# Performance work log

Measured on AMD Instinct MI355X. Metric: run time of the kernel, lower is better.

## Reference

```python
import jax, jax.numpy as jnp
import numpy as np

N, E, G, H, L, GD = 100000, 1600000, 64, 128, 3, 32
NEG_SLOPE = 0.2
EPS = 1e-5


def setup_inputs() -> dict:
    key = jax.random.key(0)
    ks = jax.random.split(key, 10)
    s = 1.0 / np.sqrt(H)
    return {
        "x": jax.random.normal(ks[0], (N, H), jnp.float32),
        "global_feat": jax.random.normal(ks[1], (G, GD), jnp.float32),
        "W_src": jax.random.normal(ks[2], (L, H, H), jnp.float32) * s,
        "W_dst": jax.random.normal(ks[3], (L, H, H), jnp.float32) * s,
        "att": jax.random.normal(ks[4], (L, H), jnp.float32) * s,
        "b_conv": jnp.zeros((L, H), jnp.float32),
        "gn_w": jnp.ones((L, H), jnp.float32),
        "gn_b": jnp.zeros((L, H), jnp.float32),
        "gn_ms": jnp.ones((L, H), jnp.float32),
        "W1": jax.random.normal(ks[5], (H * L + GD, H), jnp.float32) * (1.0 / np.sqrt(H * L + GD)),
        "b1": jnp.zeros((H,), jnp.float32),
        "W2": jax.random.normal(ks[6], (H, 1), jnp.float32) * s,
        "b2": jnp.zeros((1,), jnp.float32),
        "edge_index": jax.random.randint(ks[7], (2, E), 0, N, jnp.int64),
        "batch": jnp.sort(jax.random.randint(ks[8], (N,), 0, G, jnp.int64)),
    }


def reference(x, global_feat, W_src, W_dst, att, b_conv, gn_w, gn_b, gn_ms,
              W1, b1, W2, b2, edge_index, batch):
    n = x.shape[0]
    g = global_feat.shape[0]
    layers = W_src.shape[0]
    loops = jnp.arange(n, dtype=edge_index.dtype)
    src = jnp.concatenate([edge_index[0], loops])  # add_self_loops=True
    dst = jnp.concatenate([edge_index[1], loops])
    counts = jnp.maximum(
        jax.ops.segment_sum(jnp.ones((n,), x.dtype), batch, num_segments=g), 1.0)

    outs = []
    for l in range(layers):
        # --- GATv2Conv (heads=1) ---
        xl = x @ W_src[l]          # source transform [N,H]
        xr = x @ W_dst[l]          # target transform [N,H]
        e = jax.nn.leaky_relu(xl[src] + xr[dst], NEG_SLOPE) @ att[l]  # [Etot]
        emax = jax.ops.segment_max(e, dst, num_segments=n)
        ex = jnp.exp(e - emax[dst])
        denom = jax.ops.segment_sum(ex, dst, num_segments=n)
        alpha = ex / denom[dst]
        h = jax.ops.segment_sum(alpha[:, None] * xl[src], dst, num_segments=n) + b_conv[l]
        # --- GraphNorm ---
        mean = jax.ops.segment_sum(h, batch, num_segments=g) / counts[:, None]
        sub = h - gn_ms[l] * mean[batch]
        var = jax.ops.segment_sum(sub * sub, batch, num_segments=g) / counts[:, None]
        h = gn_w[l] * sub * jax.lax.rsqrt(var[batch] + EPS) + gn_b[l]
        x = jax.nn.relu(h)
        # --- global_mean_pool ---
        outs.append(jax.ops.segment_sum(x, batch, num_segments=g) / counts[:, None])

    hcat = jnp.concatenate(outs + [global_feat], axis=1)  # JK cat + global feats
    z = jax.nn.relu(hcat @ W1 + b1)  # dropout = identity (eval)
    return z @ W2 + b2
```

## Files before the change

### kernel.cpp

```cpp
#include <hip/hip_runtime.h>
#include <hip/hip_bf16.h>
#include <math.h>

#define N_    100000
#define E_    1600000
#define ETOT_ 1700000
#define G_    64
#define H_    128
#define GH_   8192
#define L_    3
#define GD_   32
#define NEG_  0.2f
#define EPS_  1e-5f

#define NBUK_ 391
#define CH_   2048
#define MCH_  782

typedef unsigned short ushort_t;
typedef unsigned int uint_t;
typedef __attribute__((ext_vector_type(4))) float f32x4;
typedef __attribute__((ext_vector_type(8))) short bf16x8;
typedef __attribute__((ext_vector_type(8))) unsigned short ushort8;

__device__ __forceinline__ ushort_t bfb(float f) {
    __hip_bfloat16 h = __float2bfloat16(f);
    return *reinterpret_cast<ushort_t*>(&h);
}
__device__ __forceinline__ uint_t pack_bf2(float a, float b) {
    return (uint_t)bfb(a) | ((uint_t)bfb(b) << 16);
}
__device__ __forceinline__ float uf(ushort_t u) {
    return __uint_as_float(((uint_t)u) << 16);
}


__global__ void k_init(float* pooled, float* gsum, float* gsq, int* gstart,
                       const int* __restrict__ batch,
                       const float* __restrict__ Ws, const float* __restrict__ Wd,
                       ushort_t* __restrict__ Wt) {
    int i = blockIdx.x * 256 + threadIdx.x;
    if (i < L_ * GH_) { pooled[i] = 0.f; gsum[i] = 0.f; gsq[i] = 0.f; }
    if (i <= G_) {
        int lo = 0, hi = N_;
        while (lo < hi) { int mid = (lo + hi) >> 1; if (batch[mid] < i) lo = mid + 1; else hi = mid; }
        gstart[i] = lo;
    }
    if (i < L_ * 256 * H_) {
        int l = i >> 15;
        int r = i & 32767;
        int c = r >> 7, k = r & 127;
        float v = (c < H_) ? Ws[(size_t)l * H_ * H_ + k * H_ + c]
                           : Wd[(size_t)l * H_ * H_ + k * H_ + (c - H_)];
        Wt[i] = bfb(v);
    }
}


__global__ __launch_bounds__(256) void k_bcount(const int* __restrict__ edst, int* __restrict__ C) {
    __shared__ int hist[NBUK_];
    int t = threadIdx.x, m = blockIdx.x;
    for (int i = t; i < NBUK_; i += 256) hist[i] = 0;
    __syncthreads();
    int base = m * CH_;
#pragma unroll
    for (int j = 0; j < CH_ / 256; j++) {
        int e = base + j * 256 + t;
        if (e < E_) atomicAdd(&hist[edst[e] >> 8], 1);
    }
    __syncthreads();
    for (int i = t; i < NBUK_; i += 256) C[i * MCH_ + m] = hist[i];
}

__global__ __launch_bounds__(1024) void k_bscan(int* __restrict__ C, int* __restrict__ bucketEdges) {
    __shared__ int arr[1024];
    int b = blockIdx.x, t = threadIdx.x;
    int v = (t < MCH_) ? C[b * MCH_ + t] : 0;
    arr[t] = v;
    __syncthreads();
    for (int off = 1; off < 1024; off <<= 1) {
        int x = (t >= off) ? arr[t - off] : 0;
        __syncthreads();
        arr[t] += x;
        __syncthreads();
    }
    if (t < MCH_) C[b * MCH_ + t] = arr[t] - v;
    if (t == 1023) bucketEdges[b] = arr[1023];
}

__global__ __launch_bounds__(512) void k_bscan2(const int* __restrict__ bucketEdges,
                                                int* __restrict__ bstartE, int* __restrict__ bstartT,
                                                int* __restrict__ rowptr) {
    __shared__ int aE[512], aT[512];
    int t = threadIdx.x;
    int e = 0, tot = 0;
    if (t < NBUK_) {
        e = bucketEdges[t];
        int nib = N_ - t * 256; if (nib > 256) nib = 256;
        tot = e + nib;
    }
    aE[t] = e; aT[t] = tot;
    __syncthreads();
    for (int off = 1; off < 512; off <<= 1) {
        int xe = (t >= off) ? aE[t - off] : 0;
        int xt = (t >= off) ? aT[t - off] : 0;
        __syncthreads();
        aE[t] += xe; aT[t] += xt;
        __syncthreads();
    }
    if (t < NBUK_) { bstartE[t] = aE[t] - e; bstartT[t] = aT[t] - tot; }
    if (t == 0) rowptr[N_] = ETOT_;
}

__global__ __launch_bounds__(256) void k_bscatter(const int* __restrict__ esrc, const int* __restrict__ edst,
                                                  const int* __restrict__ C, const int* __restrict__ bstartE,
                                                  uint_t* __restrict__ stag) {
    __shared__ int cur[NBUK_];
    int t = threadIdx.x, m = blockIdx.x;
    for (int i = t; i < NBUK_; i += 256) cur[i] = C[i * MCH_ + m] + bstartE[i];
    __syncthreads();
    int base = m * CH_;
#pragma unroll
    for (int j = 0; j < CH_ / 256; j++) {
        int e = base + j * 256 + t;
        if (e < E_) {
            int s = esrc[e], d = edst[e];
            int pos = atomicAdd(&cur[d >> 8], 1);
            stag[pos] = ((uint_t)s << 8) | (uint_t)(d & 255);
        }
    }
}

__global__ __launch_bounds__(256) void k_bfinal(const uint_t* __restrict__ stag,
                                                const int* __restrict__ bucketEdges,
                                                const int* __restrict__ bstartE, const int* __restrict__ bstartT,
                                                int* __restrict__ rowptr, int* __restrict__ colarr) {
    __shared__ int deg[256];
    __shared__ int cursor[256];
    int b = blockIdx.x, t = threadIdx.x;
    int nb0 = b * 256;
    int nib = N_ - nb0; if (nib > 256) nib = 256;
    int ebeg = bstartE[b], ecnt = bucketEdges[b];
    deg[t] = (t < nib) ? 1 : 0;
    __syncthreads();
    for (int i = t; i < ecnt; i += 256) {
        uint_t p = stag[ebeg + i];
        atomicAdd(&deg[p & 255u], 1);
    }
    __syncthreads();
    int v = deg[t];
    cursor[t] = v;
    __syncthreads();
    for (int off = 1; off < 256; off <<= 1) {
        int x = (t >= off) ? cursor[t - off] : 0;
        __syncthreads();
        cursor[t] += x;
        __syncthreads();
    }
    int excl = cursor[t] - v;
    int rowbase = bstartT[b];
    if (t < nib) {
        rowptr[nb0 + t] = rowbase + excl;
        colarr[rowbase + excl] = nb0 + t;
    }
    __syncthreads();
    cursor[t] = excl + 1;
    __syncthreads();
    for (int i = t; i < ecnt; i += 256) {
        uint_t p = stag[ebeg + i];
        int pos = atomicAdd(&cursor[p & 255u], 1);
        colarr[rowbase + pos] = (int)(p >> 8);
    }
}


template<int FIRST>
__global__ __launch_bounds__(256) void k_mfma_t(const float* __restrict__ x0,
                                                const ushort_t* __restrict__ hin,
                                                const int* __restrict__ batch,
                                                const float* __restrict__ mv,
                                                const float* __restrict__ iv,
                                                const float* __restrict__ bb,
                                                const ushort_t* __restrict__ Wt,
                                                ushort_t* __restrict__ xlb,
                                                ushort_t* __restrict__ xrb) {
    int wv = threadIdx.x >> 6, lane = threadIdx.x & 63;
    int row0 = (blockIdx.x * 4 + wv) * 16;
    if (row0 >= N_) return;
    int sl = lane & 15, q = lane >> 4;
    int row = row0 + sl;

    bf16x8 bx[4];
    if (FIRST) {
        const float* ap = x0 + (size_t)row * H_ + q * 8;
#pragma unroll
        for (int kk = 0; kk < 4; kk++) {
            float4 v0 = *(const float4*)(ap + kk * 32);
            float4 v1 = *(const float4*)(ap + kk * 32 + 4);
            bf16x8 t;
            t[0] = (short)bfb(v0.x); t[1] = (short)bfb(v0.y);
            t[2] = (short)bfb(v0.z); t[3] = (short)bfb(v0.w);
            t[4] = (short)bfb(v1.x); t[5] = (short)bfb(v1.y);
            t[6] = (short)bfb(v1.z); t[7] = (short)bfb(v1.w);
            bx[kk] = t;
        }
    } else {
        int g = batch[row];
        const ushort_t* hp = hin + (size_t)row * H_ + q * 8;
        const float* mvp = mv + g * H_ + q * 8;
        const float* ivp = iv + g * H_ + q * 8;
        const float* bbp = bb + q * 8;
#pragma unroll
        for (int kk = 0; kk < 4; kk++) {
            ushort8 u = *(const ushort8*)(hp + kk * 32);
            float4 m0 = *(const float4*)(mvp + kk * 32);
            float4 m1 = *(const float4*)(mvp + kk * 32 + 4);
            float4 i0 = *(const float4*)(ivp + kk * 32);
            float4 i1 = *(const float4*)(ivp + kk * 32 + 4);
            float4 c0 = *(const float4*)(bbp + kk * 32);
            float4 c1 = *(const float4*)(bbp + kk * 32 + 4);
            bf16x8 t;
            t[0] = (short)bfb(fmaxf((uf(u[0]) - m0.x) * i0.x + c0.x, 0.f));
            t[1] = (short)bfb(fmaxf((uf(u[1]) - m0.y) * i0.y + c0.y, 0.f));
            t[2] = (short)bfb(fmaxf((uf(u[2]) - m0.z) * i0.z + c0.z, 0.f));
            t[3] = (short)bfb(fmaxf((uf(u[3]) - m0.w) * i0.w + c0.w, 0.f));
            t[4] = (short)bfb(fmaxf((uf(u[4]) - m1.x) * i1.x + c1.x, 0.f));
            t[5] = (short)bfb(fmaxf((uf(u[5]) - m1.y) * i1.y + c1.y, 0.f));
            t[6] = (short)bfb(fmaxf((uf(u[6]) - m1.z) * i1.z + c1.z, 0.f));
            t[7] = (short)bfb(fmaxf((uf(u[7]) - m1.w) * i1.w + c1.w, 0.f));
            bx[kk] = t;
        }
    }

    f32x4 acc[16];
#pragma unroll
    for (int c = 0; c < 16; c++) acc[c] = (f32x4){0.f, 0.f, 0.f, 0.f};

#pragma unroll
    for (int c = 0; c < 16; c++) {
        const ushort_t* wp = Wt + (size_t)(c * 16 + sl) * H_ + q * 8;
#pragma unroll
        for (int kk = 0; kk < 4; kk++) {
            bf16x8 aw = *(const bf16x8*)(wp + kk * 32);
            acc[c] = __builtin_amdgcn_mfma_f32_16x16x32_bf16(aw, bx[kk], acc[c], 0, 0, 0);
        }
    }

    ushort_t* xlp = xlb + (size_t)row * H_ + q * 4;
    ushort_t* xrp = xrb + (size_t)row * H_ + q * 4;
#pragma unroll
    for (int c = 0; c < 8; c++) {
        uint2 o;
        o.x = pack_bf2(acc[c][0], acc[c][1]);
        o.y = pack_bf2(acc[c][2], acc[c][3]);
        *(uint2*)(xlp + c * 16) = o;
    }
#pragma unroll
    for (int c = 8; c < 16; c++) {
        uint2 o;
        o.x = pack_bf2(acc[c][0], acc[c][1]);
        o.y = pack_bf2(acc[c][2], acc[c][3]);
        *(uint2*)(xrp + (c - 8) * 16) = o;
    }
}


__global__ __launch_bounds__(256) void k_conv(const ushort_t* __restrict__ xlb,
                                              const ushort_t* __restrict__ xrb,
                                              const int* __restrict__ rowptr,
                                              const int* __restrict__ colarr,
                                              const float* __restrict__ attl, const float* __restrict__ bcl,
                                              ushort_t* __restrict__ h) {
    int tid = threadIdx.x;
    int lane = tid & 63, wv = tid >> 6;
    int sl = lane & 15, q = lane >> 4;
    int row = blockIdx.x * 16 + wv * 4 + q;
    int d0 = sl * 8;

    float xrv[8], av[8], av5[8];
    {
        ushort8 ux = *(const ushort8*)(xrb + (size_t)row * H_ + d0);
        float4 a0 = *(const float4*)(attl + d0);
        float4 a1 = *(const float4*)(attl + d0 + 4);
        av[0] = a0.x; av[1] = a0.y; av[2] = a0.z; av[3] = a0.w;
        av[4] = a1.x; av[5] = a1.y; av[6] = a1.z; av[7] = a1.w;
#pragma unroll
        for (int e = 0; e < 8; e++) { xrv[e] = uf(ux[e]); av5[e] = NEG_ * av[e]; }
    }

    int jb = rowptr[row];
    int n = rowptr[row + 1] - jb;

    float ssum0 = 0.f, ssum1 = 0.f;
    float ac0[8] = {0.f, 0.f, 0.f, 0.f, 0.f, 0.f, 0.f, 0.f};
    float ac1[8] = {0.f, 0.f, 0.f, 0.f, 0.f, 0.f, 0.f, 0.f};

    auto PROC = [&](const ushort8& u, float& ss, float* acm) {
        float v[8];
        float p = 0.f;
#pragma unroll
        for (int e = 0; e < 8; e++) {
            v[e] = uf(u[e]);
            float t = v[e] + xrv[e];
            p = fmaf(t, (t > 0.f ? av[e] : av5[e]), p);
        }
        p += __shfl_xor(p, 8);
        p += __shfl_xor(p, 4);
        p += __shfl_xor(p, 2);
        p += __shfl_xor(p, 1);
        float wgt = __expf(p);
        ss += wgt;
#pragma unroll
        for (int e = 0; e < 8; e++) acm[e] = fmaf(wgt, v[e], acm[e]);
    };

    int cA = colarr[jb];
    ushort8 uA = *(const ushort8*)(xlb + (size_t)cA * H_ + d0);
    int cB = colarr[jb + (n > 1 ? 1 : 0)];
    ushort8 uB = *(const ushort8*)(xlb + (size_t)cB * H_ + d0);

    int i = 0;
    for (; i + 2 < n; i += 2) {
        int cC = colarr[jb + i + 2];
        int cD = colarr[jb + (i + 3 < n ? i + 3 : i + 2)];
        PROC(uA, ssum0, ac0);
        uA = *(const ushort8*)(xlb + (size_t)cC * H_ + d0);
        PROC(uB, ssum1, ac1);
        uB = *(const ushort8*)(xlb + (size_t)cD * H_ + d0);
    }
    PROC(uA, ssum0, ac0);
    if (i + 1 < n) PROC(uB, ssum1, ac1);

    float inv = 1.f / (ssum0 + ssum1);
    float4 b0 = *(const float4*)(bcl + d0);
    float4 b1 = *(const float4*)(bcl + d0 + 4);
    ushort8 ho;
    ho[0] = bfb((ac0[0] + ac1[0]) * inv + b0.x); ho[1] = bfb((ac0[1] + ac1[1]) * inv + b0.y);
    ho[2] = bfb((ac0[2] + ac1[2]) * inv + b0.z); ho[3] = bfb((ac0[3] + ac1[3]) * inv + b0.w);
    ho[4] = bfb((ac0[4] + ac1[4]) * inv + b1.x); ho[5] = bfb((ac0[5] + ac1[5]) * inv + b1.y);
    ho[6] = bfb((ac0[6] + ac1[6]) * inv + b1.z); ho[7] = bfb((ac0[7] + ac1[7]) * inv + b1.w);
    *(ushort8*)(h + (size_t)row * H_ + d0) = ho;
}


__global__ void k_gn_stat(const ushort_t* __restrict__ h, const int* __restrict__ batch,
                          float* gsum, float* gsq) {
    int tid = threadIdx.x;
    int nb = blockIdx.x * 64;
    int d2 = (tid & 63) * 2, hh = tid >> 6;
    int nend = nb + 64; if (nend > N_) nend = N_;
    float s10 = 0.f, s11 = 0.f, s20 = 0.f, s21 = 0.f; int curg = -1;
    for (int n = nb + hh; n < nend; n += 4) {
        int g = batch[n];
        if (g != curg) {
            if (curg >= 0) {
                atomicAdd(&gsum[curg * H_ + d2], s10);
                atomicAdd(&gsum[curg * H_ + d2 + 1], s11);
                atomicAdd(&gsq[curg * H_ + d2], s20);
                atomicAdd(&gsq[curg * H_ + d2 + 1], s21);
            }
            s10 = s11 = s20 = s21 = 0.f; curg = g;
        }
        uint_t u = *(const uint_t*)(h + (size_t)n * H_ + d2);
        float v0 = __uint_as_float(u << 16);
        float v1 = __uint_as_float(u & 0xffff0000u);
        s10 += v0; s11 += v1; s20 += v0 * v0; s21 += v1 * v1;
    }
    if (curg >= 0) {
        atomicAdd(&gsum[curg * H_ + d2], s10);
        atomicAdd(&gsum[curg * H_ + d2 + 1], s11);
        atomicAdd(&gsq[curg * H_ + d2], s20);
        atomicAdd(&gsq[curg * H_ + d2 + 1], s21);
    }
}


__global__ void k_gn_fin(float* gsum, float* gsq, const int* __restrict__ gstart,
                         const float* __restrict__ gnwl, const float* __restrict__ gnmsl) {
    int i = blockIdx.x * 256 + threadIdx.x;
    if (i < GH_) {
        int g = i >> 7, d = i & 127;
        int c = gstart[g + 1] - gstart[g]; if (c < 1) c = 1;
        float ic = 1.f / (float)c;
        float mean = gsum[i] * ic;
        float e2   = gsq[i] * ic;
        float ms = gnmsl[d];
        float var = e2 - ms * (2.f - ms) * mean * mean;
        gsum[i] = ms * mean;
        gsq[i]  = gnwl[d] * rsqrtf(var + EPS_);
    }
}


__global__ void k_pool(const ushort_t* __restrict__ h, const int* __restrict__ batch,
                       const float* __restrict__ mv, const float* __restrict__ iv,
                       const float* __restrict__ bb, float* __restrict__ pooled_l) {
    int tid = threadIdx.x;
    int nb = blockIdx.x * 64;
    int d2 = (tid & 63) * 2, hh = tid >> 6;
    int nend = nb + 64; if (nend > N_) nend = N_;
    float b0 = bb[d2], b1 = bb[d2 + 1];
    float p0 = 0.f, p1 = 0.f; int curg = -1;
    float m0 = 0.f, m1 = 0.f, i0 = 0.f, i1 = 0.f;
    for (int n = nb + hh; n < nend; n += 4) {
        int g = batch[n];
        if (g != curg) {
            if (curg >= 0) {
                atomicAdd(&pooled_l[curg * H_ + d2], p0);
                atomicAdd(&pooled_l[curg * H_ + d2 + 1], p1);
            }
            p0 = 0.f; p1 = 0.f; curg = g;
            m0 = mv[g * H_ + d2]; m1 = mv[g * H_ + d2 + 1];
            i0 = iv[g * H_ + d2]; i1 = iv[g * H_ + d2 + 1];
        }
        uint_t u = *(const uint_t*)(h + (size_t)n * H_ + d2);
        float v0 = __uint_as_float(u << 16);
        float v1 = __uint_as_float(u & 0xffff0000u);
        v0 = fmaxf((v0 - m0) * i0 + b0, 0.f);
        v1 = fmaxf((v1 - m1) * i1 + b1, 0.f);
        p0 += v0; p1 += v1;
    }
    if (curg >= 0) {
        atomicAdd(&pooled_l[curg * H_ + d2], p0);
        atomicAdd(&pooled_l[curg * H_ + d2 + 1], p1);
    }
}


__global__ __launch_bounds__(128) void k_mlp(const float* __restrict__ pooled, const float* __restrict__ gfeat,
                                             const int* __restrict__ gstart,
                                             const float* __restrict__ W1, const float* __restrict__ b1,
                                             const float* __restrict__ W2, const float* __restrict__ b2,
                                             float* __restrict__ out) {
    int g = blockIdx.x;
    int c = threadIdx.x;
    __shared__ float hc[H_ * L_ + GD_];
    __shared__ float zz[H_];
    int cn = gstart[g + 1] - gstart[g]; if (cn < 1) cn = 1;
    float ic = 1.f / (float)cn;
    for (int k = c; k < H_ * L_; k += 128)
        hc[k] = pooled[(k >> 7) * GH_ + g * H_ + (k & 127)] * ic;
    if (c < GD_) hc[H_ * L_ + c] = gfeat[g * GD_ + c];
    __syncthreads();
    float z = b1[c];
#pragma unroll 4
    for (int k = 0; k < H_ * L_ + GD_; k++)
        z += hc[k] * W1[k * H_ + c];
    z = fmaxf(z, 0.f);
    zz[c] = z * W2[c];
    __syncthreads();
    for (int off = 64; off > 0; off >>= 1) {
        if (c < off) zz[c] += zz[c + off];
        __syncthreads();
    }
    if (c == 0) out[g] = zz[0] + b2[0];
}


extern "C" void kernel_launch(void* const* d_in, const int* in_sizes, int n_in,
                              void* d_out, int out_size, void* d_ws, size_t ws_size,
                              hipStream_t stream) {
    const float* x0    = (const float*)d_in[0];
    const float* gfeat = (const float*)d_in[1];
    const float* Wsrc  = (const float*)d_in[2];
    const float* Wdst  = (const float*)d_in[3];
    const float* att   = (const float*)d_in[4];
    const float* bconv = (const float*)d_in[5];
    const float* gnw   = (const float*)d_in[6];
    const float* gnb   = (const float*)d_in[7];
    const float* gnms  = (const float*)d_in[8];
    const float* W1    = (const float*)d_in[9];
    const float* b1    = (const float*)d_in[10];
    const float* W2    = (const float*)d_in[11];
    const float* b2    = (const float*)d_in[12];
    const int*   eidx  = (const int*)d_in[13];
    const int*   batch = (const int*)d_in[14];
    const int* esrc = eidx;
    const int* edst = eidx + E_;
    float* out = (float*)d_out;

    char* w = (char*)d_ws;
    size_t off = 0;
    auto alloc = [&](size_t bytes) { char* p = w + off; off += (bytes + 255) & ~(size_t)255; return p; };
    ushort_t* xlb  = (ushort_t*)alloc((size_t)N_ * H_ * 2);
    ushort_t* xrb  = (ushort_t*)alloc((size_t)N_ * H_ * 2);
    ushort_t* h    = (ushort_t*)alloc((size_t)N_ * H_ * 2);
    ushort_t* Wt   = (ushort_t*)alloc((size_t)L_ * 256 * H_ * 2);
    int*   rowptr  = (int*)alloc((size_t)(N_ + 1) * 4);
    int*   colarr  = (int*)alloc((size_t)ETOT_ * 4);
    int*   bktE    = (int*)alloc(NBUK_ * 4);
    int*   bstartE = (int*)alloc(NBUK_ * 4);
    int*   bstartT = (int*)alloc(NBUK_ * 4);
    int*   gstart  = (int*)alloc((G_ + 1) * 4);
    float* gsum    = (float*)alloc((size_t)L_ * GH_ * 4);
    float* gsq     = (float*)alloc((size_t)L_ * GH_ * 4);
    float* pooled  = (float*)alloc((size_t)L_ * GH_ * 4);
    uint_t* stag = (uint_t*)xlb;
    int*    C    = (int*)xrb;
    (void)ws_size; (void)in_sizes; (void)n_in; (void)out_size;

    k_init<<<(N_ + 255) / 256, 256, 0, stream>>>(pooled, gsum, gsq, gstart, batch,
                                                 Wsrc, Wdst, Wt);
    k_bcount<<<MCH_, 256, 0, stream>>>(edst, C);
    k_bscan<<<NBUK_, 1024, 0, stream>>>(C, bktE);
    k_bscan2<<<1, 512, 0, stream>>>(bktE, bstartE, bstartT, rowptr);
    k_bscatter<<<MCH_, 256, 0, stream>>>(esrc, edst, C, bstartE, stag);
    k_bfinal<<<NBUK_, 256, 0, stream>>>(stag, bktE, bstartE, bstartT, rowptr, colarr);

    int mfma_grid = (N_ / 16 + 3) / 4;
    for (int l = 0; l < L_; l++) {
        if (l == 0)
            k_mfma_t<1><<<mfma_grid, 256, 0, stream>>>(x0, h, batch, gsum, gsq, gnb,
                                                       Wt, xlb, xrb);
        else
            k_mfma_t<0><<<mfma_grid, 256, 0, stream>>>(x0, h, batch,
                                                       gsum + (size_t)(l - 1) * GH_,
                                                       gsq + (size_t)(l - 1) * GH_,
                                                       gnb + (size_t)(l - 1) * H_,
                                                       Wt + (size_t)l * 256 * H_, xlb, xrb);
        k_conv<<<N_ / 16, 256, 0, stream>>>(xlb, xrb, rowptr, colarr,
                                            att + (size_t)l * H_, bconv + (size_t)l * H_, h);
        k_gn_stat<<<(N_ + 63) / 64, 256, 0, stream>>>(h, batch,
                                                      gsum + (size_t)l * GH_, gsq + (size_t)l * GH_);
        k_gn_fin<<<GH_ / 256, 256, 0, stream>>>(gsum + (size_t)l * GH_, gsq + (size_t)l * GH_,
                                                gstart, gnw + (size_t)l * H_, gnms + (size_t)l * H_);
        k_pool<<<(N_ + 63) / 64, 256, 0, stream>>>(h, batch,
                                                   gsum + (size_t)l * GH_, gsq + (size_t)l * GH_,
                                                   gnb + (size_t)l * H_, pooled + (size_t)l * GH_);
    }

    k_mlp<<<G_, 128, 0, stream>>>(pooled, gfeat, gstart, W1, b1, W2, b2, out);
}
```

Measured before the change: 684.2 us.

## Switch intermediates to fp16 and use packed half math in the edge conv

Stores the projected features, the weights and the conv output in fp16 instead of bf16, and uses f16 MFMA for the projection. The edge-attention kernel now does leaky-relu, attention dot product and weighted accumulation with packed fp16 vector arithmetic instead of per-element fp32. Its two-accumulator unrolled gather is replaced by a single-accumulator loop with a three-deep software prefetch. This cuts ALU work per edge, but accumulating in fp16 risks precision loss and overflow, and the single accumulator lengthens the dependency chain.

```diff
diff --git a/kernel.cpp b/kernel.cpp
--- a/kernel.cpp
+++ b/kernel.cpp
@@ -1,5 +1,4 @@
 #include <hip/hip_runtime.h>
-#include <hip/hip_bf16.h>
 #include <math.h>
 
 #define N_    100000
@@ -19,19 +18,19 @@
 
 typedef unsigned short ushort_t;
 typedef unsigned int uint_t;
+typedef _Float16 half_t;
 typedef __attribute__((ext_vector_type(4))) float f32x4;
-typedef __attribute__((ext_vector_type(8))) short bf16x8;
-typedef __attribute__((ext_vector_type(8))) unsigned short ushort8;
-
-__device__ __forceinline__ ushort_t bfb(float f) {
-    __hip_bfloat16 h = __float2bfloat16(f);
+typedef __attribute__((ext_vector_type(2))) _Float16 h2;
+typedef __attribute__((ext_vector_type(8))) _Float16 f16x8;
+
+__device__ __forceinline__ ushort_t hbits(float f) {
+    half_t h = (half_t)f;
     return *reinterpret_cast<ushort_t*>(&h);
 }
-__device__ __forceinline__ uint_t pack_bf2(float a, float b) {
-    return (uint_t)bfb(a) | ((uint_t)bfb(b) << 16);
-}
-__device__ __forceinline__ float uf(ushort_t u) {
-    return __uint_as_float(((uint_t)u) << 16);
+__device__ __forceinline__ uint_t pack_h2(float a, float b) {
+    half_t ha = (half_t)a, hb = (half_t)b;
+    return (uint_t)*reinterpret_cast<ushort_t*>(&ha) |
+           ((uint_t)*reinterpret_cast<ushort_t*>(&hb) << 16);
 }
 
 
@@ -52,7 +51,7 @@
         int c = r >> 7, k = r & 127;
         float v = (c < H_) ? Ws[(size_t)l * H_ * H_ + k * H_ + c]
                            : Wd[(size_t)l * H_ * H_ + k * H_ + (c - H_)];
-        Wt[i] = bfb(v);
+        Wt[i] = hbits(v);
     }
 }
 
@@ -190,18 +189,18 @@
     int sl = lane & 15, q = lane >> 4;
     int row = row0 + sl;
 
-    bf16x8 bx[4];
+    f16x8 bx[4];
     if (FIRST) {
         const float* ap = x0 + (size_t)row * H_ + q * 8;
 #pragma unroll
         for (int kk = 0; kk < 4; kk++) {
             float4 v0 = *(const float4*)(ap + kk * 32);
             float4 v1 = *(const float4*)(ap + kk * 32 + 4);
-            bf16x8 t;
-            t[0] = (short)bfb(v0.x); t[1] = (short)bfb(v0.y);
-            t[2] = (short)bfb(v0.z); t[3] = (short)bfb(v0.w);
-            t[4] = (short)bfb(v1.x); t[5] = (short)bfb(v1.y);
-            t[6] = (short)bfb(v1.z); t[7] = (short)bfb(v1.w);
+            f16x8 t;
+            t[0] = (half_t)v0.x; t[1] = (half_t)v0.y;
+            t[2] = (half_t)v0.z; t[3] = (half_t)v0.w;
+            t[4] = (half_t)v1.x; t[5] = (half_t)v1.y;
+            t[6] = (half_t)v1.z; t[7] = (half_t)v1.w;
             bx[kk] = t;
         }
     } else {
@@ -212,22 +211,22 @@
         const float* bbp = bb + q * 8;
 #pragma unroll
         for (int kk = 0; kk < 4; kk++) {
-            ushort8 u = *(const ushort8*)(hp + kk * 32);
+            f16x8 u = *(const f16x8*)(hp + kk * 32);
             float4 m0 = *(const float4*)(mvp + kk * 32);
             float4 m1 = *(const float4*)(mvp + kk * 32 + 4);
             float4 i0 = *(const float4*)(ivp + kk * 32);
             float4 i1 = *(const float4*)(ivp + kk * 32 + 4);
             float4 c0 = *(const float4*)(bbp + kk * 32);
             float4 c1 = *(const float4*)(bbp + kk * 32 + 4);
-            bf16x8 t;
-            t[0] = (short)bfb(fmaxf((uf(u[0]) - m0.x) * i0.x + c0.x, 0.f));
-            t[1] = (short)bfb(fmaxf((uf(u[1]) - m0.y) * i0.y + c0.y, 0.f));
-            t[2] = (short)bfb(fmaxf((uf(u[2]) - m0.z) * i0.z + c0.z, 0.f));
-            t[3] = (short)bfb(fmaxf((uf(u[3]) - m0.w) * i0.w + c0.w, 0.f));
-            t[4] = (short)bfb(fmaxf((uf(u[4]) - m1.x) * i1.x + c1.x, 0.f));
-            t[5] = (short)bfb(fmaxf((uf(u[5]) - m1.y) * i1.y + c1.y, 0.f));
-            t[6] = (short)bfb(fmaxf((uf(u[6]) - m1.z) * i1.z + c1.z, 0.f));
-            t[7] = (short)bfb(fmaxf((uf(u[7]) - m1.w) * i1.w + c1.w, 0.f));
+            f16x8 t;
+            t[0] = (half_t)fmaxf(((float)u[0] - m0.x) * i0.x + c0.x, 0.f);
+            t[1] = (half_t)fmaxf(((float)u[1] - m0.y) * i0.y + c0.y, 0.f);
+            t[2] = (half_t)fmaxf(((float)u[2] - m0.z) * i0.z + c0.z, 0.f);
+            t[3] = (half_t)fmaxf(((float)u[3] - m0.w) * i0.w + c0.w, 0.f);
+            t[4] = (half_t)fmaxf(((float)u[4] - m1.x) * i1.x + c1.x, 0.f);
+            t[5] = (half_t)fmaxf(((float)u[5] - m1.y) * i1.y + c1.y, 0.f);
+            t[6] = (half_t)fmaxf(((float)u[6] - m1.z) * i1.z + c1.z, 0.f);
+            t[7] = (half_t)fmaxf(((float)u[7] - m1.w) * i1.w + c1.w, 0.f);
             bx[kk] = t;
         }
     }
@@ -241,8 +240,8 @@
         const ushort_t* wp = Wt + (size_t)(c * 16 + sl) * H_ + q * 8;
 #pragma unroll
         for (int kk = 0; kk < 4; kk++) {
-            bf16x8 aw = *(const bf16x8*)(wp + kk * 32);
-            acc[c] = __builtin_amdgcn_mfma_f32_16x16x32_bf16(aw, bx[kk], acc[c], 0, 0, 0);
+            f16x8 aw = *(const f16x8*)(wp + kk * 32);
+            acc[c] = __builtin_amdgcn_mfma_f32_16x16x32_f16(aw, bx[kk], acc[c], 0, 0, 0);
         }
     }
 
@@ -251,15 +250,15 @@
 #pragma unroll
     for (int c = 0; c < 8; c++) {
         uint2 o;
-        o.x = pack_bf2(acc[c][0], acc[c][1]);
-        o.y = pack_bf2(acc[c][2], acc[c][3]);
+        o.x = pack_h2(acc[c][0], acc[c][1]);
+        o.y = pack_h2(acc[c][2], acc[c][3]);
         *(uint2*)(xlp + c * 16) = o;
     }
 #pragma unroll
     for (int c = 8; c < 16; c++) {
         uint2 o;
-        o.x = pack_bf2(acc[c][0], acc[c][1]);
-        o.y = pack_bf2(acc[c][2], acc[c][3]);
+        o.x = pack_h2(acc[c][0], acc[c][1]);
+        o.y = pack_h2(acc[c][2], acc[c][3]);
         *(uint2*)(xrp + (c - 8) * 16) = o;
     }
 }
@@ -277,69 +276,64 @@
     int row = blockIdx.x * 16 + wv * 4 + q;
     int d0 = sl * 8;
 
-    float xrv[8], av[8], av5[8];
+    const half_t neg = (half_t)NEG_;
+    f16x8 xr8 = *(const f16x8*)(xrb + (size_t)row * H_ + d0);
+    f16x8 at8;
     {
-        ushort8 ux = *(const ushort8*)(xrb + (size_t)row * H_ + d0);
         float4 a0 = *(const float4*)(attl + d0);
         float4 a1 = *(const float4*)(attl + d0 + 4);
-        av[0] = a0.x; av[1] = a0.y; av[2] = a0.z; av[3] = a0.w;
-        av[4] = a1.x; av[5] = a1.y; av[6] = a1.z; av[7] = a1.w;
-#pragma unroll
-        for (int e = 0; e < 8; e++) { xrv[e] = uf(ux[e]); av5[e] = NEG_ * av[e]; }
+        at8[0] = (half_t)a0.x; at8[1] = (half_t)a0.y;
+        at8[2] = (half_t)a0.z; at8[3] = (half_t)a0.w;
+        at8[4] = (half_t)a1.x; at8[5] = (half_t)a1.y;
+        at8[6] = (half_t)a1.z; at8[7] = (half_t)a1.w;
     }
 
     int jb = rowptr[row];
     int n = rowptr[row + 1] - jb;
-
-    float ssum0 = 0.f, ssum1 = 0.f;
-    float ac0[8] = {0.f, 0.f, 0.f, 0.f, 0.f, 0.f, 0.f, 0.f};
-    float ac1[8] = {0.f, 0.f, 0.f, 0.f, 0.f, 0.f, 0.f, 0.f};
-
-    auto PROC = [&](const ushort8& u, float& ss, float* acm) {
-        float v[8];
-        float p = 0.f;
-#pragma unroll
-        for (int e = 0; e < 8; e++) {
-            v[e] = uf(u[e]);
-            float t = v[e] + xrv[e];
-            p = fmaf(t, (t > 0.f ? av[e] : av5[e]), p);
-        }
+    int last = n - 1;
+
+    float ssum = 0.f;
+    f16x8 ac8 = (f16x8)(half_t)0.f;
+
+    auto PROC = [&](f16x8 v8) {
+        f16x8 t8 = v8 + xr8;
+        f16x8 r8 = __builtin_elementwise_max(t8, t8 * neg);
+        f16x8 q8 = r8 * at8;
+        h2 s2 = __builtin_shufflevector(q8, q8, 0, 1) + __builtin_shufflevector(q8, q8, 2, 3)
+              + __builtin_shufflevector(q8, q8, 4, 5) + __builtin_shufflevector(q8, q8, 6, 7);
+        float p = (float)s2[0] + (float)s2[1];
         p += __shfl_xor(p, 8);
         p += __shfl_xor(p, 4);
         p += __shfl_xor(p, 2);
         p += __shfl_xor(p, 1);
         float wgt = __expf(p);
-        ss += wgt;
-#pragma unroll
-        for (int e = 0; e < 8; e++) acm[e] = fmaf(wgt, v[e], acm[e]);
+        ssum += wgt;
+        ac8 += v8 * (half_t)wgt;
     };
 
-    int cA = colarr[jb];
-    ushort8 uA = *(const ushort8*)(xlb + (size_t)cA * H_ + d0);
-    int cB = colarr[jb + (n > 1 ? 1 : 0)];
-    ushort8 uB = *(const ushort8*)(xlb + (size_t)cB * H_ + d0);
-
-    int i = 0;
-    for (; i + 2 < n; i += 2) {
-        int cC = colarr[jb + i + 2];
-        int cD = colarr[jb + (i + 3 < n ? i + 3 : i + 2)];
-        PROC(uA, ssum0, ac0);
-        uA = *(const ushort8*)(xlb + (size_t)cC * H_ + d0);
-        PROC(uB, ssum1, ac1);
-        uB = *(const ushort8*)(xlb + (size_t)cD * H_ + d0);
-    }
-    PROC(uA, ssum0, ac0);
-    if (i + 1 < n) PROC(uB, ssum1, ac1);
-
-    float inv = 1.f / (ssum0 + ssum1);
+    int c0 = colarr[jb];
+    int c1 = colarr[jb + (1 < last ? 1 : last)];
+    int sc = colarr[jb + (2 < last ? 2 : last)];
+    f16x8 u0 = *(const f16x8*)(xlb + (size_t)c0 * H_ + d0);
+    f16x8 u1 = *(const f16x8*)(xlb + (size_t)c1 * H_ + d0);
+
+    for (int i = 0; i < n; i++) {
+        int i3 = i + 3; if (i3 > last) i3 = last;
+        int cn = colarr[jb + i3];
+        f16x8 u2 = *(const f16x8*)(xlb + (size_t)sc * H_ + d0);
+        PROC(u0);
+        u0 = u1; u1 = u2; sc = cn;
+    }
+
+    float inv = 1.f / ssum;
     float4 b0 = *(const float4*)(bcl + d0);
     float4 b1 = *(const float4*)(bcl + d0 + 4);
-    ushort8 ho;
-    ho[0] = bfb((ac0[0] + ac1[0]) * inv + b0.x); ho[1] = bfb((ac0[1] + ac1[1]) * inv + b0.y);
-    ho[2] = bfb((ac0[2] + ac1[2]) * inv + b0.z); ho[3] = bfb((ac0[3] + ac1[3]) * inv + b0.w);
-    ho[4] = bfb((ac0[4] + ac1[4]) * inv + b1.x); ho[5] = bfb((ac0[5] + ac1[5]) * inv + b1.y);
-    ho[6] = bfb((ac0[6] + ac1[6]) * inv + b1.z); ho[7] = bfb((ac0[7] + ac1[7]) * inv + b1.w);
-    *(ushort8*)(h + (size_t)row * H_ + d0) = ho;
+    f16x8 ho;
+    ho[0] = (half_t)((float)ac8[0] * inv + b0.x); ho[1] = (half_t)((float)ac8[1] * inv + b0.y);
+    ho[2] = (half_t)((float)ac8[2] * inv + b0.z); ho[3] = (half_t)((float)ac8[3] * inv + b0.w);
+    ho[4] = (half_t)((float)ac8[4] * inv + b1.x); ho[5] = (half_t)((float)ac8[5] * inv + b1.y);
+    ho[6] = (half_t)((float)ac8[6] * inv + b1.z); ho[7] = (half_t)((float)ac8[7] * inv + b1.w);
+    *(f16x8*)(h + (size_t)row * H_ + d0) = ho;
 }
 
 
@@ -361,9 +355,9 @@
             }
             s10 = s11 = s20 = s21 = 0.f; curg = g;
         }
-        uint_t u = *(const uint_t*)(h + (size_t)n * H_ + d2);
-        float v0 = __uint_as_float(u << 16);
-        float v1 = __uint_as_float(u & 0xffff0000u);
+        h2 u = *(const h2*)(h + (size_t)n * H_ + d2);
+        float v0 = (float)u[0];
+        float v1 = (float)u[1];
         s10 += v0; s11 += v1; s20 += v0 * v0; s21 += v1 * v1;
     }
     if (curg >= 0) {
@@ -413,11 +407,9 @@
             m0 = mv[g * H_ + d2]; m1 = mv[g * H_ + d2 + 1];
             i0 = iv[g * H_ + d2]; i1 = iv[g * H_ + d2 + 1];
         }
-        uint_t u = *(const uint_t*)(h + (size_t)n * H_ + d2);
-        float v0 = __uint_as_float(u << 16);
-        float v1 = __uint_as_float(u & 0xffff0000u);
-        v0 = fmaxf((v0 - m0) * i0 + b0, 0.f);
-        v1 = fmaxf((v1 - m1) * i1 + b1, 0.f);
+        h2 u = *(const h2*)(h + (size_t)n * H_ + d2);
+        float v0 = fmaxf(((float)u[0] - m0) * i0 + b0, 0.f);
+        float v1 = fmaxf(((float)u[1] - m1) * i1 + b1, 0.f);
         p0 += v0; p1 += v1;
     }
     if (curg >= 0) {
```

Result: no change. 687.6 us (+0.5%).

## Fuse GraphNorm finalize and mean-pool into next layer's transform kernel

Applied to the files above, without the earlier changes.

Removes the k_gn_fin kernel and computes GraphNorm mean and inverse std inline from the raw sums in both the transform and pool kernels. For layers 1 and 2 the global mean pool of the previous layer is folded into the next layer's MFMA kernel, using shared-memory reduction when a block falls within one graph and direct global atomics otherwise, so only the final layer keeps a separate pool launch. The conv kernel's gather loop is also restructured from two interleaved accumulators into a single accumulator with a three-deep software prefetch. This saves two launches and one full read of h per layer, but adds rsqrt work per element and LDS atomics, and pooling now uses bf16-rounded activations.

```diff
diff --git a/kernel.cpp b/kernel.cpp
--- a/kernel.cpp
+++ b/kernel.cpp
@@ -178,20 +178,27 @@
 __global__ __launch_bounds__(256) void k_mfma_t(const float* __restrict__ x0,
                                                 const ushort_t* __restrict__ hin,
                                                 const int* __restrict__ batch,
-                                                const float* __restrict__ mv,
-                                                const float* __restrict__ iv,
-                                                const float* __restrict__ bb,
+                                                const float* __restrict__ gsum,
+                                                const float* __restrict__ gsq,
+                                                const int* __restrict__ gstart,
+                                                const float* __restrict__ gnwl,
+                                                const float* __restrict__ gnmsl,
+                                                const float* __restrict__ bbl,
                                                 const ushort_t* __restrict__ Wt,
                                                 ushort_t* __restrict__ xlb,
-                                                ushort_t* __restrict__ xrb) {
-    int wv = threadIdx.x >> 6, lane = threadIdx.x & 63;
+                                                ushort_t* __restrict__ xrb,
+                                                float* __restrict__ pooled_prev) {
+    __shared__ float ps[H_];
+    int tid = threadIdx.x;
+    int wv = tid >> 6, lane = tid & 63;
     int row0 = (blockIdx.x * 4 + wv) * 16;
-    if (row0 >= N_) return;
+    bool active = row0 < N_;
     int sl = lane & 15, q = lane >> 4;
-    int row = row0 + sl;
+    int row = active ? row0 + sl : 0;
 
     bf16x8 bx[4];
     if (FIRST) {
+        if (!active) return;
         const float* ap = x0 + (size_t)row * H_ + q * 8;
 #pragma unroll
         for (int kk = 0; kk < 4; kk++) {
@@ -206,28 +213,41 @@
         }
     } else {
         int g = batch[row];
+        float cnt = (float)(gstart[g + 1] - gstart[g]); if (cnt < 1.f) cnt = 1.f;
+        float ic = 1.f / cnt;
         const ushort_t* hp = hin + (size_t)row * H_ + q * 8;
-        const float* mvp = mv + g * H_ + q * 8;
-        const float* ivp = iv + g * H_ + q * 8;
-        const float* bbp = bb + q * 8;
+        const float* gsp = gsum + g * H_ + q * 8;
+        const float* gqp = gsq  + g * H_ + q * 8;
+        const float* msp = gnmsl + q * 8;
+        const float* gwp = gnwl + q * 8;
+        const float* bbp = bbl + q * 8;
 #pragma unroll
         for (int kk = 0; kk < 4; kk++) {
             ushort8 u = *(const ushort8*)(hp + kk * 32);
-            float4 m0 = *(const float4*)(mvp + kk * 32);
-            float4 m1 = *(const float4*)(mvp + kk * 32 + 4);
-            float4 i0 = *(const float4*)(ivp + kk * 32);
-            float4 i1 = *(const float4*)(ivp + kk * 32 + 4);
+            float4 s0 = *(const float4*)(gsp + kk * 32);
+            float4 s1 = *(const float4*)(gsp + kk * 32 + 4);
+            float4 e0 = *(const float4*)(gqp + kk * 32);
+            float4 e1 = *(const float4*)(gqp + kk * 32 + 4);
+            float4 m0 = *(const float4*)(msp + kk * 32);
+            float4 m1 = *(const float4*)(msp + kk * 32 + 4);
+            float4 w0 = *(const float4*)(gwp + kk * 32);
+            float4 w1 = *(const float4*)(gwp + kk * 32 + 4);
             float4 c0 = *(const float4*)(bbp + kk * 32);
             float4 c1 = *(const float4*)(bbp + kk * 32 + 4);
+            float sv[8] = { s0.x, s0.y, s0.z, s0.w, s1.x, s1.y, s1.z, s1.w };
+            float ev[8] = { e0.x, e0.y, e0.z, e0.w, e1.x, e1.y, e1.z, e1.w };
+            float mv[8] = { m0.x, m0.y, m0.z, m0.w, m1.x, m1.y, m1.z, m1.w };
+            float wv8[8] = { w0.x, w0.y, w0.z, w0.w, w1.x, w1.y, w1.z, w1.w };
+            float bv[8] = { c0.x, c0.y, c0.z, c0.w, c1.x, c1.y, c1.z, c1.w };
             bf16x8 t;
-            t[0] = (short)bfb(fmaxf((uf(u[0]) - m0.x) * i0.x + c0.x, 0.f));
-            t[1] = (short)bfb(fmaxf((uf(u[1]) - m0.y) * i0.y + c0.y, 0.f));
-            t[2] = (short)bfb(fmaxf((uf(u[2]) - m0.z) * i0.z + c0.z, 0.f));
-            t[3] = (short)bfb(fmaxf((uf(u[3]) - m0.w) * i0.w + c0.w, 0.f));
-            t[4] = (short)bfb(fmaxf((uf(u[4]) - m1.x) * i1.x + c1.x, 0.f));
-            t[5] = (short)bfb(fmaxf((uf(u[5]) - m1.y) * i1.y + c1.y, 0.f));
-            t[6] = (short)bfb(fmaxf((uf(u[6]) - m1.z) * i1.z + c1.z, 0.f));
-            t[7] = (short)bfb(fmaxf((uf(u[7]) - m1.w) * i1.w + c1.w, 0.f));
+#pragma unroll
+            for (int e = 0; e < 8; e++) {
+                float mean = sv[e] * ic;
+                float var = ev[e] * ic - mv[e] * (2.f - mv[e]) * mean * mean;
+                float iv = wv8[e] * rsqrtf(var + EPS_);
+                float y = fmaxf((uf(u[e]) - mv[e] * mean) * iv + bv[e], 0.f);
+                t[e] = (short)bfb(y);
+            }
             bx[kk] = t;
         }
     }
@@ -246,21 +266,51 @@
         }
     }
 
-    ushort_t* xlp = xlb + (size_t)row * H_ + q * 4;
-    ushort_t* xrp = xrb + (size_t)row * H_ + q * 4;
-#pragma unroll
-    for (int c = 0; c < 8; c++) {
-        uint2 o;
-        o.x = pack_bf2(acc[c][0], acc[c][1]);
-        o.y = pack_bf2(acc[c][2], acc[c][3]);
-        *(uint2*)(xlp + c * 16) = o;
-    }
-#pragma unroll
-    for (int c = 8; c < 16; c++) {
-        uint2 o;
-        o.x = pack_bf2(acc[c][0], acc[c][1]);
-        o.y = pack_bf2(acc[c][2], acc[c][3]);
-        *(uint2*)(xrp + (c - 8) * 16) = o;
+    if (active) {
+        ushort_t* xlp = xlb + (size_t)row * H_ + q * 4;
+        ushort_t* xrp = xrb + (size_t)row * H_ + q * 4;
+#pragma unroll
+        for (int c = 0; c < 8; c++) {
+            uint2 o;
+            o.x = pack_bf2(acc[c][0], acc[c][1]);
+            o.y = pack_bf2(acc[c][2], acc[c][3]);
+            *(uint2*)(xlp + c * 16) = o;
+        }
+#pragma unroll
+        for (int c = 8; c < 16; c++) {
+            uint2 o;
+            o.x = pack_bf2(acc[c][0], acc[c][1]);
+            o.y = pack_bf2(acc[c][2], acc[c][3]);
+            *(uint2*)(xrp + (c - 8) * 16) = o;
+        }
+    }
+
+    if (!FIRST) {
+        if (tid < H_) ps[tid] = 0.f;
+        __syncthreads();
+        int rb = blockIdx.x * 64;
+        int rl = rb + 63; if (rl > N_ - 1) rl = N_ - 1;
+        int ga = batch[rb], gb = batch[rl];
+        if (ga == gb) {
+            if (active) {
+#pragma unroll
+                for (int kk = 0; kk < 4; kk++)
+#pragma unroll
+                    for (int e = 0; e < 8; e++)
+                        atomicAdd(&ps[q * 8 + kk * 32 + e], uf((ushort_t)bx[kk][e]));
+            }
+            __syncthreads();
+            if (tid < H_) atomicAdd(&pooled_prev[ga * H_ + tid], ps[tid]);
+        } else {
+            if (active) {
+                int g2 = batch[row];
+#pragma unroll
+                for (int kk = 0; kk < 4; kk++)
+#pragma unroll
+                    for (int e = 0; e < 8; e++)
+                        atomicAdd(&pooled_prev[g2 * H_ + q * 8 + kk * 32 + e], uf((ushort_t)bx[kk][e]));
+            }
+        }
     }
 }
 
@@ -290,17 +340,27 @@
 
     int jb = rowptr[row];
     int n = rowptr[row + 1] - jb;
-
-    float ssum0 = 0.f, ssum1 = 0.f;
-    float ac0[8] = {0.f, 0.f, 0.f, 0.f, 0.f, 0.f, 0.f, 0.f};
-    float ac1[8] = {0.f, 0.f, 0.f, 0.f, 0.f, 0.f, 0.f, 0.f};
-
-    auto PROC = [&](const ushort8& u, float& ss, float* acm) {
+    int last = n - 1;
+
+    float ssum = 0.f;
+    float ac[8] = {0.f, 0.f, 0.f, 0.f, 0.f, 0.f, 0.f, 0.f};
+
+    int c0 = colarr[jb];
+    int c1 = colarr[jb + (1 < last ? 1 : last)];
+    int sc = colarr[jb + (2 < last ? 2 : last)];
+    ushort8 u0 = *(const ushort8*)(xlb + (size_t)c0 * H_ + d0);
+    ushort8 u1 = *(const ushort8*)(xlb + (size_t)c1 * H_ + d0);
+
+    for (int i = 0; i < n; i++) {
+        int i3 = i + 3; if (i3 > last) i3 = last;
+        int cn = colarr[jb + i3];
+        ushort8 u2 = *(const ushort8*)(xlb + (size_t)sc * H_ + d0);
+
         float v[8];
         float p = 0.f;
 #pragma unroll
         for (int e = 0; e < 8; e++) {
-            v[e] = uf(u[e]);
+            v[e] = uf(u0[e]);
             float t = v[e] + xrv[e];
             p = fmaf(t, (t > 0.f ? av[e] : av5[e]), p);
         }
@@ -309,36 +369,21 @@
         p += __shfl_xor(p, 2);
         p += __shfl_xor(p, 1);
         float wgt = __expf(p);
-        ss += wgt;
-#pragma unroll
-        for (int e = 0; e < 8; e++) acm[e] = fmaf(wgt, v[e], acm[e]);
-    };
-
-    int cA = colarr[jb];
-    ushort8 uA = *(const ushort8*)(xlb + (size_t)cA * H_ + d0);
-    int cB = colarr[jb + (n > 1 ? 1 : 0)];
-    ushort8 uB = *(const ushort8*)(xlb + (size_t)cB * H_ + d0);
-
-    int i = 0;
-    for (; i + 2 < n; i += 2) {
-        int cC = colarr[jb + i + 2];
-        int cD = colarr[jb + (i + 3 < n ? i + 3 : i + 2)];
-        PROC(uA, ssum0, ac0);
-        uA = *(const ushort8*)(xlb + (size_t)cC * H_ + d0);
-        PROC(uB, ssum1, ac1);
-        uB = *(const ushort8*)(xlb + (size_t)cD * H_ + d0);
-    }
-    PROC(uA, ssum0, ac0);
-    if (i + 1 < n) PROC(uB, ssum1, ac1);
-
-    float inv = 1.f / (ssum0 + ssum1);
+        ssum += wgt;
+#pragma unroll
+        for (int e = 0; e < 8; e++) ac[e] = fmaf(wgt, v[e], ac[e]);
+
+        u0 = u1; u1 = u2; sc = cn;
+    }
+
+    float inv = 1.f / ssum;
     float4 b0 = *(const float4*)(bcl + d0);
     float4 b1 = *(const float4*)(bcl + d0 + 4);
     ushort8 ho;
-    ho[0] = bfb((ac0[0] + ac1[0]) * inv + b0.x); ho[1] = bfb((ac0[1] + ac1[1]) * inv + b0.y);
-    ho[2] = bfb((ac0[2] + ac1[2]) * inv + b0.z); ho[3] = bfb((ac0[3] + ac1[3]) * inv + b0.w);
-    ho[4] = bfb((ac0[4] + ac1[4]) * inv + b1.x); ho[5] = bfb((ac0[5] + ac1[5]) * inv + b1.y);
-    ho[6] = bfb((ac0[6] + ac1[6]) * inv + b1.z); ho[7] = bfb((ac0[7] + ac1[7]) * inv + b1.w);
+    ho[0] = bfb(ac[0] * inv + b0.x); ho[1] = bfb(ac[1] * inv + b0.y);
+    ho[2] = bfb(ac[2] * inv + b0.z); ho[3] = bfb(ac[3] * inv + b0.w);
+    ho[4] = bfb(ac[4] * inv + b1.x); ho[5] = bfb(ac[5] * inv + b1.y);
+    ho[6] = bfb(ac[6] * inv + b1.z); ho[7] = bfb(ac[7] * inv + b1.w);
     *(ushort8*)(h + (size_t)row * H_ + d0) = ho;
 }
 
@@ -375,31 +420,18 @@
 }
 
 
-__global__ void k_gn_fin(float* gsum, float* gsq, const int* __restrict__ gstart,
-                         const float* __restrict__ gnwl, const float* __restrict__ gnmsl) {
-    int i = blockIdx.x * 256 + threadIdx.x;
-    if (i < GH_) {
-        int g = i >> 7, d = i & 127;
-        int c = gstart[g + 1] - gstart[g]; if (c < 1) c = 1;
-        float ic = 1.f / (float)c;
-        float mean = gsum[i] * ic;
-        float e2   = gsq[i] * ic;
-        float ms = gnmsl[d];
-        float var = e2 - ms * (2.f - ms) * mean * mean;
-        gsum[i] = ms * mean;
-        gsq[i]  = gnwl[d] * rsqrtf(var + EPS_);
-    }
-}
-
-
 __global__ void k_pool(const ushort_t* __restrict__ h, const int* __restrict__ batch,
-                       const float* __restrict__ mv, const float* __restrict__ iv,
+                       const float* __restrict__ gsum, const float* __restrict__ gsq,
+                       const int* __restrict__ gstart,
+                       const float* __restrict__ gnwl, const float* __restrict__ gnmsl,
                        const float* __restrict__ bb, float* __restrict__ pooled_l) {
     int tid = threadIdx.x;
     int nb = blockIdx.x * 64;
     int d2 = (tid & 63) * 2, hh = tid >> 6;
     int nend = nb + 64; if (nend > N_) nend = N_;
     float b0 = bb[d2], b1 = bb[d2 + 1];
+    float ms0 = gnmsl[d2], ms1 = gnmsl[d2 + 1];
+    float w0 = gnwl[d2], w1 = gnwl[d2 + 1];
     float p0 = 0.f, p1 = 0.f; int curg = -1;
     float m0 = 0.f, m1 = 0.f, i0 = 0.f, i1 = 0.f;
     for (int n = nb + hh; n < nend; n += 4) {
@@ -410,8 +442,14 @@
                 atomicAdd(&pooled_l[curg * H_ + d2 + 1], p1);
             }
             p0 = 0.f; p1 = 0.f; curg = g;
-            m0 = mv[g * H_ + d2]; m1 = mv[g * H_ + d2 + 1];
-            i0 = iv[g * H_ + d2]; i1 = iv[g * H_ + d2 + 1];
+            float cnt = (float)(gstart[g + 1] - gstart[g]); if (cnt < 1.f) cnt = 1.f;
+            float ic = 1.f / cnt;
+            float mean0 = gsum[g * H_ + d2] * ic;
+            float mean1 = gsum[g * H_ + d2 + 1] * ic;
+            float var0 = gsq[g * H_ + d2] * ic - ms0 * (2.f - ms0) * mean0 * mean0;
+            float var1 = gsq[g * H_ + d2 + 1] * ic - ms1 * (2.f - ms1) * mean1 * mean1;
+            m0 = ms0 * mean0; m1 = ms1 * mean1;
+            i0 = w0 * rsqrtf(var0 + EPS_); i1 = w1 * rsqrtf(var1 + EPS_);
         }
         uint_t u = *(const uint_t*)(h + (size_t)n * H_ + d2);
         float v0 = __uint_as_float(u << 16);
@@ -510,24 +548,30 @@
     int mfma_grid = (N_ / 16 + 3) / 4;
     for (int l = 0; l < L_; l++) {
         if (l == 0)
-            k_mfma_t<1><<<mfma_grid, 256, 0, stream>>>(x0, h, batch, gsum, gsq, gnb,
-                                                       Wt, xlb, xrb);
+            k_mfma_t<1><<<mfma_grid, 256, 0, stream>>>(x0, h, batch,
+                                                       gsum, gsq, gstart, gnw, gnms, gnb,
+                                                       Wt, xlb, xrb, pooled);
         else
             k_mfma_t<0><<<mfma_grid, 256, 0, stream>>>(x0, h, batch,
                                                        gsum + (size_t)(l - 1) * GH_,
                                                        gsq + (size_t)(l - 1) * GH_,
+                                                       gstart,
+                                                       gnw + (size_t)(l - 1) * H_,
+                                                       gnms + (size_t)(l - 1) * H_,
                                                        gnb + (size_t)(l - 1) * H_,
-                                                       Wt + (size_t)l * 256 * H_, xlb, xrb);
+                                                       Wt + (size_t)l * 256 * H_, xlb, xrb,
+                                                       pooled + (size_t)(l - 1) * GH_);
         k_conv<<<N_ / 16, 256, 0, stream>>>(xlb, xrb, rowptr, colarr,
                                             att + (size_t)l * H_, bconv + (size_t)l * H_, h);
         k_gn_stat<<<(N_ + 63) / 64, 256, 0, stream>>>(h, batch,
                                                       gsum + (size_t)l * GH_, gsq + (size_t)l * GH_);
-        k_gn_fin<<<GH_ / 256, 256, 0, stream>>>(gsum + (size_t)l * GH_, gsq + (size_t)l * GH_,
-                                                gstart, gnw + (size_t)l * H_, gnms + (size_t)l * H_);
-        k_pool<<<(N_ + 63) / 64, 256, 0, stream>>>(h, batch,
-                                                   gsum + (size_t)l * GH_, gsq + (size_t)l * GH_,
-                                                   gnb + (size_t)l * H_, pooled + (size_t)l * GH_);
-    }
+    }
+
+    k_pool<<<(N_ + 63) / 64, 256, 0, stream>>>(h, batch,
+                                               gsum + (size_t)2 * GH_, gsq + (size_t)2 * GH_,
+                                               gstart,
+                                               gnw + (size_t)2 * H_, gnms + (size_t)2 * H_,
+                                               gnb + (size_t)2 * H_, pooled + (size_t)2 * GH_);
 
     k_mlp<<<G_, 128, 0, stream>>>(pooled, gfeat, gstart, W1, b1, W2, b2, out);
 }
```

Result: slower. 899.6 us (+31.5%).
